# Kernel tuning notes

Hardware: AMD Instinct MI355X
Metric: run time of the kernel (lower is better)

The kernel has to match this reference:

```python
import jax, jax.numpy as jnp
import numpy as np

N, E, DN, DE, H = 50000, 800000, 64, 64, 128


def setup_inputs() -> dict:
    key = jax.random.key(0)
    ks = jax.random.split(key, 12)
    s = 0.05
    return {
        "h": jax.random.normal(ks[0], (N, DN), jnp.float32),
        "eh": jax.random.normal(ks[1], (E, DE), jnp.float32),
        "W_node1": jax.random.normal(ks[2], (DN, H), jnp.float32) * s,
        "b_node1": jax.random.normal(ks[3], (H,), jnp.float32) * s,
        "W_node2": jax.random.normal(ks[4], (H, H), jnp.float32) * s,
        "W_edge1": jax.random.normal(ks[5], (DE, H), jnp.float32) * s,
        "b_edge1": jax.random.normal(ks[6], (H,), jnp.float32) * s,
        "W_edge2": jax.random.normal(ks[7], (H, H), jnp.float32) * s,
        "W_comb": jax.random.normal(ks[8], (H, DN), jnp.float32) * s,
        "W_ue": jax.random.normal(ks[9], (DN, DE), jnp.float32) * s,
        "src": jax.random.randint(ks[10], (E,), 0, N, jnp.int32),
        "dst": jax.random.randint(ks[11], (E,), 0, N, jnp.int32),
    }


def reference(h, eh, W_node1, b_node1, W_node2, W_edge1, b_edge1, W_edge2, W_comb, W_ue, src, dst):
    # gather per-edge endpoint node features: [E, DN]
    hs = h[src]
    hd = h[dst]
    # edge update: h_e = 0.8*h_e + 0.2 * fc_update_edge(h_src * h_dst)
    eh_new = 0.8 * eh + 0.2 * ((hs * hd) @ W_ue)
    # message: two small MLPs then tanh-combine, all per edge
    m1 = jax.nn.relu(hs @ W_node1 + b_node1) @ W_node2       # [E, H]
    m2 = jax.nn.relu(eh_new @ W_edge1 + b_edge1) @ W_edge2   # [E, H]
    m = jnp.tanh((m1 * m2) @ W_comb)                          # [E, DN]
    # reduce: scatter-sum messages to destination nodes + residual
    agg = jax.ops.segment_sum(m, dst, num_segments=h.shape[0])
    return agg + h
```

## Files before the change

### kernel.cpp

```cpp
#include <hip/hip_runtime.h>
#include <hip/hip_bf16.h>

#define NN 50000
#define NE 800000
#define DNODE 64
#define HD 128

typedef __attribute__((ext_vector_type(8)))  short bf16x8;
typedef __attribute__((ext_vector_type(16))) float f32x16;
typedef __attribute__((ext_vector_type(4)))  float f32x4;

__device__ __forceinline__ short f2bf(float f) {
    __hip_bfloat16 b = __float2bfloat16(f);
    unsigned short u;
    __builtin_memcpy(&u, &b, 2);
    return (short)u;
}
__device__ __forceinline__ float bf2f(short s) {
    return __uint_as_float(((unsigned)(unsigned short)s) << 16);
}
__device__ __forceinline__ f32x16 zero16() {
    f32x16 z;
#pragma unroll
    for (int i = 0; i < 16; ++i) z[i] = 0.f;
    return z;
}

__device__ __forceinline__ void build_frags(const float* __restrict__ W, int ncols,
                                            int nks, int nct, bf16x8* dst,
                                            int tid, int nthr) {
    int total = nct * nks * 64;
    for (int p = tid; p < total; p += nthr) {
        int fi = p >> 6, l = p & 63;
        int ct = fi / nks, ks = fi - ct * nks;
        int col = 32 * ct + (l & 31);
        int kb  = 16 * ks + 8 * (l >> 5);
        bf16x8 v;
#pragma unroll
        for (int j = 0; j < 8; ++j) v[j] = f2bf(W[(size_t)(kb + j) * ncols + col]);
        dst[p] = v;
    }
}

__global__ __launch_bounds__(512, 2) void node_kernel(
        const float* __restrict__ h, const float* __restrict__ Wn1,
        const float* __restrict__ bn1, const float* __restrict__ Wn2,
        unsigned short* __restrict__ M1, float* __restrict__ out, int ntiles) {
    __shared__ bf16x8 fWn1[16 * 64];
    __shared__ bf16x8 fWn2[32 * 64];
    __shared__ float  bias[HD];
    __shared__ __align__(16) char stg[8][8192];

    int tid = threadIdx.x;
    build_frags(Wn1, HD, 4, 4, fWn1, tid, 512);
    build_frags(Wn2, HD, 8, 4, fWn2, tid, 512);
    if (tid < HD) bias[tid] = bn1[tid];
    __syncthreads();

    int wv = tid >> 6, lane = tid & 63;
    int la = lane & 31, hh = lane >> 5;
    char* stage = stg[wv];

    float bv[4];
#pragma unroll
    for (int ct = 0; ct < 4; ++ct) bv[ct] = bias[32 * ct + la];

    int tile = blockIdx.x * 8 + wv;
    if (tile >= ntiles) return;
    int n0 = tile * 32;
    int nd = n0 + la;
    int ndc = nd < NN ? nd : NN - 1;

    f32x16 accT[4] = {zero16(), zero16(), zero16(), zero16()};
#pragma unroll
    for (int ks = 0; ks < 4; ++ks) {
        int cb = 16 * ks + 8 * hh;
        f32x4 h0 = *(const f32x4*)&h[(size_t)ndc * DNODE + cb];
        f32x4 h1 = *(const f32x4*)&h[(size_t)ndc * DNODE + cb + 4];
        if (nd < NN) {
            *(f32x4*)&out[(size_t)nd * DNODE + cb]     = h0;
            *(f32x4*)&out[(size_t)nd * DNODE + cb + 4] = h1;
        }
        bf16x8 a;
#pragma unroll
        for (int j = 0; j < 4; ++j) { a[j] = f2bf(h0[j]); a[4 + j] = f2bf(h1[j]); }
#pragma unroll
        for (int ct = 0; ct < 4; ++ct)
            accT[ct] = __builtin_amdgcn_mfma_f32_32x32x16_bf16(a, fWn1[(ct * 4 + ks) * 64 + lane], accT[ct], 0, 0, 0);
    }
#pragma unroll
    for (int ct = 0; ct < 4; ++ct)
#pragma unroll
        for (int r = 0; r < 16; ++r) {
            int row = (r & 3) + 8 * (r >> 2) + 4 * hh;
            float v = fmaxf(accT[ct][r] + bv[ct], 0.f);
            int col = 32 * ct + la;
            *(short*)&stage[row * 256 + ((2 * col) ^ ((row & 7) << 4))] = f2bf(v);
        }
    f32x16 accM[4] = {zero16(), zero16(), zero16(), zero16()};
#pragma unroll
    for (int ks = 0; ks < 8; ++ks) {
        int k0 = 16 * ks + 8 * hh;
        bf16x8 a = *(const bf16x8*)&stage[la * 256 + ((2 * k0) ^ ((la & 7) << 4))];
#pragma unroll
        for (int ct = 0; ct < 4; ++ct)
            accM[ct] = __builtin_amdgcn_mfma_f32_32x32x16_bf16(a, fWn2[(ct * 8 + ks) * 64 + lane], accM[ct], 0, 0, 0);
    }
#pragma unroll
    for (int ct = 0; ct < 4; ++ct)
#pragma unroll
        for (int r = 0; r < 16; ++r) {
            int row = (r & 3) + 8 * (r >> 2) + 4 * hh;
            int node = n0 + row;
            if (node < NN)
                M1[(size_t)node * HD + 32 * ct + la] = (unsigned short)f2bf(accM[ct][r]);
        }
}

__global__ __launch_bounds__(512, 2) void edge_kernel(
        const float* __restrict__ h, const float* __restrict__ eh,
        const float* __restrict__ Wue, const float* __restrict__ We1,
        const float* __restrict__ be1, const float* __restrict__ We2,
        const float* __restrict__ Wcb, const int* __restrict__ src,
        const int* __restrict__ dst, const unsigned short* __restrict__ M1,
        float* __restrict__ out) {
    __shared__ bf16x8 fUe[8 * 64];
    __shared__ bf16x8 fE1[16 * 64];
    __shared__ bf16x8 fE2[32 * 64];
    __shared__ bf16x8 fCb[16 * 64];
    __shared__ float  bias[HD];
    __shared__ __align__(16) char stg[8][8192];
    __shared__ int    sdd[8][32];

    int tid = threadIdx.x;
    build_frags(Wue, 64, 4, 2, fUe, tid, 512);
    build_frags(We1, HD, 4, 4, fE1, tid, 512);
    build_frags(We2, HD, 8, 4, fE2, tid, 512);
    build_frags(Wcb, 64, 8, 2, fCb, tid, 512);
    if (tid < HD) bias[tid] = be1[tid];
    __syncthreads();

    int wv = tid >> 6, lane = tid & 63;
    int la = lane & 31, hh = lane >> 5;
    char* stage = stg[wv];

    float bv[4];
#pragma unroll
    for (int ct = 0; ct < 4; ++ct) bv[ct] = bias[32 * ct + la];

    const int NT = NE / 32;
    int gw = blockIdx.x * 8 + wv;
    int t0 = (int)(((long long)gw * NT) >> 11);
    int t1 = (int)(((long long)(gw + 1) * NT) >> 11);

    for (int t = t0; t < t1; ++t) {
        int e0 = t * 32;
        if (lane < 32) sdd[wv][lane] = dst[e0 + lane];
        int srcA = src[e0 + la];
        int dstA = dst[e0 + la];

        int dstD[16];
#pragma unroll
        for (int r = 0; r < 16; ++r)
            dstD[r] = sdd[wv][(r & 3) + 8 * (r >> 2) + 4 * hh];

        float ehv[2][16];
#pragma unroll
        for (int ct = 0; ct < 2; ++ct)
#pragma unroll
            for (int r = 0; r < 16; ++r) {
                int row = (r & 3) + 8 * (r >> 2) + 4 * hh;
                ehv[ct][r] = eh[(size_t)(e0 + row) * 64 + 32 * ct + la];
            }

        bf16x8 mv[8];
#pragma unroll
        for (int ks = 0; ks < 8; ++ks)
            mv[ks] = *(const bf16x8*)((const char*)M1 + (size_t)srcA * 256 + 32 * ks + 16 * hh);

        f32x16 accU[2] = {zero16(), zero16()};
#pragma unroll
        for (int ks = 0; ks < 4; ++ks) {
            int cb = 16 * ks + 8 * hh;
            f32x4 s0 = *(const f32x4*)&h[(size_t)srcA * 64 + cb];
            f32x4 s1 = *(const f32x4*)&h[(size_t)srcA * 64 + cb + 4];
            f32x4 d0 = *(const f32x4*)&h[(size_t)dstA * 64 + cb];
            f32x4 d1 = *(const f32x4*)&h[(size_t)dstA * 64 + cb + 4];
            bf16x8 a;
#pragma unroll
            for (int j = 0; j < 4; ++j) {
                a[j]     = f2bf(s0[j] * d0[j]);
                a[4 + j] = f2bf(s1[j] * d1[j]);
            }
#pragma unroll
            for (int ct = 0; ct < 2; ++ct)
                accU[ct] = __builtin_amdgcn_mfma_f32_32x32x16_bf16(a, fUe[(ct * 4 + ks) * 64 + lane], accU[ct], 0, 0, 0);
        }
#pragma unroll
        for (int ct = 0; ct < 2; ++ct)
#pragma unroll
            for (int r = 0; r < 16; ++r) {
                int row = (r & 3) + 8 * (r >> 2) + 4 * hh;
                float v = 0.8f * ehv[ct][r] + 0.2f * accU[ct][r];
                int col = 32 * ct + la;
                *(short*)&stage[row * 128 + ((2 * col) ^ ((row & 7) << 4))] = f2bf(v);
            }
        f32x16 accT[4] = {zero16(), zero16(), zero16(), zero16()};
#pragma unroll
        for (int ks = 0; ks < 4; ++ks) {
            int k0 = 16 * ks + 8 * hh;
            bf16x8 a = *(const bf16x8*)&stage[la * 128 + ((2 * k0) ^ ((la & 7) << 4))];
#pragma unroll
            for (int ct = 0; ct < 4; ++ct)
                accT[ct] = __builtin_amdgcn_mfma_f32_32x32x16_bf16(a, fE1[(ct * 4 + ks) * 64 + lane], accT[ct], 0, 0, 0);
        }
#pragma unroll
        for (int ct = 0; ct < 4; ++ct)
#pragma unroll
            for (int r = 0; r < 16; ++r) {
                int row = (r & 3) + 8 * (r >> 2) + 4 * hh;
                float v = fmaxf(accT[ct][r] + bv[ct], 0.f);
                int col = 32 * ct + la;
                *(short*)&stage[row * 256 + ((2 * col) ^ ((row & 7) << 4))] = f2bf(v);
            }
        f32x16 accM[4] = {zero16(), zero16(), zero16(), zero16()};
#pragma unroll
        for (int ks = 0; ks < 8; ++ks) {
            int k0 = 16 * ks + 8 * hh;
            bf16x8 a = *(const bf16x8*)&stage[la * 256 + ((2 * k0) ^ ((la & 7) << 4))];
#pragma unroll
            for (int ct = 0; ct < 4; ++ct)
                accM[ct] = __builtin_amdgcn_mfma_f32_32x32x16_bf16(a, fE2[(ct * 8 + ks) * 64 + lane], accM[ct], 0, 0, 0);
        }
#pragma unroll
        for (int ct = 0; ct < 4; ++ct)
#pragma unroll
            for (int r = 0; r < 16; ++r) {
                int row = (r & 3) + 8 * (r >> 2) + 4 * hh;
                int col = 32 * ct + la;
                *(short*)&stage[row * 256 + ((2 * col) ^ ((row & 7) << 4))] = f2bf(accM[ct][r]);
            }
        f32x16 accF[2] = {zero16(), zero16()};
#pragma unroll
        for (int ks = 0; ks < 8; ++ks) {
            int k0 = 16 * ks + 8 * hh;
            bf16x8 m2 = *(const bf16x8*)&stage[la * 256 + ((2 * k0) ^ ((la & 7) << 4))];
            bf16x8 ap;
#pragma unroll
            for (int i = 0; i < 8; ++i)
                ap[i] = f2bf(bf2f(m2[i]) * bf2f(mv[ks][i]));
#pragma unroll
            for (int ct = 0; ct < 2; ++ct)
                accF[ct] = __builtin_amdgcn_mfma_f32_32x32x16_bf16(ap, fCb[(ct * 8 + ks) * 64 + lane], accF[ct], 0, 0, 0);
        }
#pragma unroll
        for (int ct = 0; ct < 2; ++ct)
#pragma unroll
            for (int r = 0; r < 16; ++r) {
                float x = accF[ct][r];
                x = fminf(fmaxf(x, -10.f), 10.f);
                float ex = __expf(2.f * x);
                float m = (ex - 1.f) * __builtin_amdgcn_rcpf(ex + 1.f);
                unsafeAtomicAdd(&out[(size_t)dstD[r] * 64 + 32 * ct + la], m);
            }
    }
}

extern "C" void kernel_launch(void* const* d_in, const int* in_sizes, int n_in,
                              void* d_out, int out_size, void* d_ws, size_t ws_size,
                              hipStream_t stream) {
    const float* h   = (const float*)d_in[0];
    const float* eh  = (const float*)d_in[1];
    const float* Wn1 = (const float*)d_in[2];
    const float* bn1 = (const float*)d_in[3];
    const float* Wn2 = (const float*)d_in[4];
    const float* We1 = (const float*)d_in[5];
    const float* be1 = (const float*)d_in[6];
    const float* We2 = (const float*)d_in[7];
    const float* Wcb = (const float*)d_in[8];
    const float* Wue = (const float*)d_in[9];
    const int*   src = (const int*)d_in[10];
    const int*   dst = (const int*)d_in[11];
    float* out = (float*)d_out;
    unsigned short* M1 = (unsigned short*)d_ws;

    int ntiles = (NN + 31) / 32;
    node_kernel<<<(ntiles + 7) / 8, 512, 0, stream>>>(h, Wn1, bn1, Wn2, M1, out, ntiles);
    edge_kernel<<<256, 512, 0, stream>>>(h, eh, Wue, We1, be1, We2, Wcb, src, dst, M1, out);
}
```

Baseline: 523.5 us.

## Chain MFMA stages through registers with transposed products and permlane swaps

Drops the per-wave LDS staging buffers between MLP layers. Each layer now computes a transposed product (weights as the A operand), and the accumulator is converted straight into the next layer's B fragment using packed bf16 conversion plus v_permlane32_swap. Freeing the LDS raises the occupancy target to 4 blocks per CU, and the edge grid doubles to 512 blocks. eh and M1 are loaded in the transposed layout, and destination indices come from shuffles instead of shared memory. The risk is higher register pressure under the tighter launch bound, which could cause spills.

```diff
diff --git a/kernel.cpp b/kernel.cpp
--- a/kernel.cpp
+++ b/kernel.cpp
@@ -9,6 +9,7 @@
 typedef __attribute__((ext_vector_type(8)))  short bf16x8;
 typedef __attribute__((ext_vector_type(16))) float f32x16;
 typedef __attribute__((ext_vector_type(4)))  float f32x4;
+typedef __attribute__((ext_vector_type(4)))  unsigned short u16x4;
 
 __device__ __forceinline__ short f2bf(float f) {
     __hip_bfloat16 b = __float2bfloat16(f);
@@ -16,14 +17,32 @@
     __builtin_memcpy(&u, &b, 2);
     return (short)u;
 }
-__device__ __forceinline__ float bf2f(short s) {
-    return __uint_as_float(((unsigned)(unsigned short)s) << 16);
+__device__ __forceinline__ float bf2f(unsigned short s) {
+    return __uint_as_float(((unsigned)s) << 16);
 }
 __device__ __forceinline__ f32x16 zero16() {
     f32x16 z;
 #pragma unroll
     for (int i = 0; i < 16; ++i) z[i] = 0.f;
     return z;
+}
+
+__device__ __forceinline__ unsigned cvt_pk(float lo, float hi) {
+    unsigned r;
+    asm("v_cvt_pk_bf16_f32 %0, %1, %2" : "=v"(r) : "v"(lo), "v"(hi));
+    return r;
+}
+
+__device__ __forceinline__ bf16x8 pack_swap(const float* v) {
+    unsigned w0 = cvt_pk(v[0], v[1]);
+    unsigned w1 = cvt_pk(v[2], v[3]);
+    unsigned w2 = cvt_pk(v[4], v[5]);
+    unsigned w3 = cvt_pk(v[6], v[7]);
+    asm("v_permlane32_swap_b32 %0, %1" : "+v"(w0), "+v"(w2));
+    asm("v_permlane32_swap_b32 %0, %1" : "+v"(w1), "+v"(w3));
+    union { unsigned u[4]; bf16x8 f; } o;
+    o.u[0] = w0; o.u[1] = w1; o.u[2] = w2; o.u[3] = w3;
+    return o.f;
 }
 
 __device__ __forceinline__ void build_frags(const float* __restrict__ W, int ncols,
@@ -42,14 +61,13 @@
     }
 }
 
-__global__ __launch_bounds__(512, 2) void node_kernel(
+__global__ __launch_bounds__(512, 4) void node_kernel(
         const float* __restrict__ h, const float* __restrict__ Wn1,
         const float* __restrict__ bn1, const float* __restrict__ Wn2,
         unsigned short* __restrict__ M1, float* __restrict__ out, int ntiles) {
     __shared__ bf16x8 fWn1[16 * 64];
     __shared__ bf16x8 fWn2[32 * 64];
     __shared__ float  bias[HD];
-    __shared__ __align__(16) char stg[8][8192];
 
     int tid = threadIdx.x;
     build_frags(Wn1, HD, 4, 4, fWn1, tid, 512);
@@ -59,65 +77,67 @@
 
     int wv = tid >> 6, lane = tid & 63;
     int la = lane & 31, hh = lane >> 5;
-    char* stage = stg[wv];
-
-    float bv[4];
-#pragma unroll
-    for (int ct = 0; ct < 4; ++ct) bv[ct] = bias[32 * ct + la];
 
     int tile = blockIdx.x * 8 + wv;
     if (tile >= ntiles) return;
     int n0 = tile * 32;
-    int nd = n0 + la;
-    int ndc = nd < NN ? nd : NN - 1;
-
-    f32x16 accT[4] = {zero16(), zero16(), zero16(), zero16()};
+    int n_la = n0 + la;
+    int nc = n_la < NN ? n_la : NN - 1;
+
+    bf16x8 hfrag[4];
 #pragma unroll
     for (int ks = 0; ks < 4; ++ks) {
         int cb = 16 * ks + 8 * hh;
-        f32x4 h0 = *(const f32x4*)&h[(size_t)ndc * DNODE + cb];
-        f32x4 h1 = *(const f32x4*)&h[(size_t)ndc * DNODE + cb + 4];
-        if (nd < NN) {
-            *(f32x4*)&out[(size_t)nd * DNODE + cb]     = h0;
-            *(f32x4*)&out[(size_t)nd * DNODE + cb + 4] = h1;
-        }
-        bf16x8 a;
-#pragma unroll
-        for (int j = 0; j < 4; ++j) { a[j] = f2bf(h0[j]); a[4 + j] = f2bf(h1[j]); }
-#pragma unroll
-        for (int ct = 0; ct < 4; ++ct)
-            accT[ct] = __builtin_amdgcn_mfma_f32_32x32x16_bf16(a, fWn1[(ct * 4 + ks) * 64 + lane], accT[ct], 0, 0, 0);
-    }
-#pragma unroll
-    for (int ct = 0; ct < 4; ++ct)
-#pragma unroll
-        for (int r = 0; r < 16; ++r) {
-            int row = (r & 3) + 8 * (r >> 2) + 4 * hh;
-            float v = fmaxf(accT[ct][r] + bv[ct], 0.f);
-            int col = 32 * ct + la;
-            *(short*)&stage[row * 256 + ((2 * col) ^ ((row & 7) << 4))] = f2bf(v);
-        }
-    f32x16 accM[4] = {zero16(), zero16(), zero16(), zero16()};
-#pragma unroll
-    for (int ks = 0; ks < 8; ++ks) {
-        int k0 = 16 * ks + 8 * hh;
-        bf16x8 a = *(const bf16x8*)&stage[la * 256 + ((2 * k0) ^ ((la & 7) << 4))];
-#pragma unroll
-        for (int ct = 0; ct < 4; ++ct)
-            accM[ct] = __builtin_amdgcn_mfma_f32_32x32x16_bf16(a, fWn2[(ct * 8 + ks) * 64 + lane], accM[ct], 0, 0, 0);
-    }
-#pragma unroll
-    for (int ct = 0; ct < 4; ++ct)
+        f32x4 h0 = *(const f32x4*)&h[(size_t)nc * DNODE + cb];
+        f32x4 h1 = *(const f32x4*)&h[(size_t)nc * DNODE + cb + 4];
+        if (n_la < NN) {
+            *(f32x4*)&out[(size_t)n_la * DNODE + cb]     = h0;
+            *(f32x4*)&out[(size_t)n_la * DNODE + cb + 4] = h1;
+        }
+        union { unsigned u[4]; bf16x8 f; } xf;
+        xf.u[0] = cvt_pk(h0[0], h0[1]);
+        xf.u[1] = cvt_pk(h0[2], h0[3]);
+        xf.u[2] = cvt_pk(h1[0], h1[1]);
+        xf.u[3] = cvt_pk(h1[2], h1[3]);
+        hfrag[ks] = xf.f;
+    }
+
+    bf16x8 tfrag[8];
+#pragma unroll
+    for (int ct = 0; ct < 4; ++ct) {
+        f32x16 acc = zero16();
+#pragma unroll
+        for (int ks = 0; ks < 4; ++ks)
+            acc = __builtin_amdgcn_mfma_f32_32x32x16_bf16(fWn1[(ct * 4 + ks) * 64 + lane], hfrag[ks], acc, 0, 0, 0);
+        float vals[16];
+#pragma unroll
+        for (int m = 0; m < 4; ++m) {
+            f32x4 bv = *(const f32x4*)&bias[32 * ct + 8 * m + 4 * hh];
+#pragma unroll
+            for (int j = 0; j < 4; ++j)
+                vals[4 * m + j] = fmaxf(acc[4 * m + j] + bv[j], 0.f);
+        }
+        tfrag[2 * ct]     = pack_swap(&vals[0]);
+        tfrag[2 * ct + 1] = pack_swap(&vals[8]);
+    }
+
+#pragma unroll
+    for (int ct = 0; ct < 4; ++ct) {
+        f32x16 acc = zero16();
+#pragma unroll
+        for (int ks = 0; ks < 8; ++ks)
+            acc = __builtin_amdgcn_mfma_f32_32x32x16_bf16(tfrag[ks], fWn2[(ct * 8 + ks) * 64 + lane], acc, 0, 0, 0);
 #pragma unroll
         for (int r = 0; r < 16; ++r) {
             int row = (r & 3) + 8 * (r >> 2) + 4 * hh;
             int node = n0 + row;
             if (node < NN)
-                M1[(size_t)node * HD + 32 * ct + la] = (unsigned short)f2bf(accM[ct][r]);
-        }
-}
-
-__global__ __launch_bounds__(512, 2) void edge_kernel(
+                M1[(size_t)node * HD + 32 * ct + la] = (unsigned short)f2bf(acc[r]);
+        }
+    }
+}
+
+__global__ __launch_bounds__(512, 4) void edge_kernel(
         const float* __restrict__ h, const float* __restrict__ eh,
         const float* __restrict__ Wue, const float* __restrict__ We1,
         const float* __restrict__ be1, const float* __restrict__ We2,
@@ -129,8 +149,6 @@
     __shared__ bf16x8 fE2[32 * 64];
     __shared__ bf16x8 fCb[16 * 64];
     __shared__ float  bias[HD];
-    __shared__ __align__(16) char stg[8][8192];
-    __shared__ int    sdd[8][32];
 
     int tid = threadIdx.x;
     build_frags(Wue, 64, 4, 2, fUe, tid, 512);
@@ -142,127 +160,111 @@
 
     int wv = tid >> 6, lane = tid & 63;
     int la = lane & 31, hh = lane >> 5;
-    char* stage = stg[wv];
-
-    float bv[4];
-#pragma unroll
-    for (int ct = 0; ct < 4; ++ct) bv[ct] = bias[32 * ct + la];
 
     const int NT = NE / 32;
     int gw = blockIdx.x * 8 + wv;
-    int t0 = (int)(((long long)gw * NT) >> 11);
-    int t1 = (int)(((long long)(gw + 1) * NT) >> 11);
+    int t0 = (int)(((long long)gw * NT) >> 12);
+    int t1 = (int)(((long long)(gw + 1) * NT) >> 12);
 
     for (int t = t0; t < t1; ++t) {
         int e0 = t * 32;
-        if (lane < 32) sdd[wv][lane] = dst[e0 + lane];
-        int srcA = src[e0 + la];
-        int dstA = dst[e0 + la];
-
-        int dstD[16];
-#pragma unroll
-        for (int r = 0; r < 16; ++r)
-            dstD[r] = sdd[wv][(r & 3) + 8 * (r >> 2) + 4 * hh];
-
-        float ehv[2][16];
-#pragma unroll
-        for (int ct = 0; ct < 2; ++ct)
-#pragma unroll
-            for (int r = 0; r < 16; ++r) {
-                int row = (r & 3) + 8 * (r >> 2) + 4 * hh;
-                ehv[ct][r] = eh[(size_t)(e0 + row) * 64 + 32 * ct + la];
-            }
-
-        bf16x8 mv[8];
-#pragma unroll
-        for (int ks = 0; ks < 8; ++ks)
-            mv[ks] = *(const bf16x8*)((const char*)M1 + (size_t)srcA * 256 + 32 * ks + 16 * hh);
-
-        f32x16 accU[2] = {zero16(), zero16()};
+        int e_la = e0 + la;
+        int srcA = src[e_la];
+        int dstA = dst[e_la];
+
+        f32x16 accU0 = zero16(), accU1 = zero16();
 #pragma unroll
         for (int ks = 0; ks < 4; ++ks) {
             int cb = 16 * ks + 8 * hh;
-            f32x4 s0 = *(const f32x4*)&h[(size_t)srcA * 64 + cb];
-            f32x4 s1 = *(const f32x4*)&h[(size_t)srcA * 64 + cb + 4];
-            f32x4 d0 = *(const f32x4*)&h[(size_t)dstA * 64 + cb];
-            f32x4 d1 = *(const f32x4*)&h[(size_t)dstA * 64 + cb + 4];
-            bf16x8 a;
-#pragma unroll
-            for (int j = 0; j < 4; ++j) {
-                a[j]     = f2bf(s0[j] * d0[j]);
-                a[4 + j] = f2bf(s1[j] * d1[j]);
+            f32x4 s0 = *(const f32x4*)&h[(size_t)srcA * DNODE + cb];
+            f32x4 s1 = *(const f32x4*)&h[(size_t)srcA * DNODE + cb + 4];
+            f32x4 d0 = *(const f32x4*)&h[(size_t)dstA * DNODE + cb];
+            f32x4 d1 = *(const f32x4*)&h[(size_t)dstA * DNODE + cb + 4];
+            union { unsigned u[4]; bf16x8 f; } xf;
+            xf.u[0] = cvt_pk(s0[0] * d0[0], s0[1] * d0[1]);
+            xf.u[1] = cvt_pk(s0[2] * d0[2], s0[3] * d0[3]);
+            xf.u[2] = cvt_pk(s1[0] * d1[0], s1[1] * d1[1]);
+            xf.u[3] = cvt_pk(s1[2] * d1[2], s1[3] * d1[3]);
+            accU0 = __builtin_amdgcn_mfma_f32_32x32x16_bf16(fUe[(0 * 4 + ks) * 64 + lane], xf.f, accU0, 0, 0, 0);
+            accU1 = __builtin_amdgcn_mfma_f32_32x32x16_bf16(fUe[(1 * 4 + ks) * 64 + lane], xf.f, accU1, 0, 0, 0);
+        }
+
+        bf16x8 efrag[4];
+#pragma unroll
+        for (int ct = 0; ct < 2; ++ct) {
+            const f32x16& aU = ct ? accU1 : accU0;
+            float vals[16];
+#pragma unroll
+            for (int m = 0; m < 4; ++m) {
+                f32x4 ev = *(const f32x4*)&eh[(size_t)e_la * 64 + 32 * ct + 8 * m + 4 * hh];
+#pragma unroll
+                for (int j = 0; j < 4; ++j)
+                    vals[4 * m + j] = 0.8f * ev[j] + 0.2f * aU[4 * m + j];
             }
-#pragma unroll
-            for (int ct = 0; ct < 2; ++ct)
-                accU[ct] = __builtin_amdgcn_mfma_f32_32x32x16_bf16(a, fUe[(ct * 4 + ks) * 64 + lane], accU[ct], 0, 0, 0);
-        }
-#pragma unroll
-        for (int ct = 0; ct < 2; ++ct)
+            efrag[2 * ct]     = pack_swap(&vals[0]);
+            efrag[2 * ct + 1] = pack_swap(&vals[8]);
+        }
+
+        bf16x8 tfrag[8];
+#pragma unroll
+        for (int ct = 0; ct < 4; ++ct) {
+            f32x16 acc = zero16();
+#pragma unroll
+            for (int ks = 0; ks < 4; ++ks)
+                acc = __builtin_amdgcn_mfma_f32_32x32x16_bf16(fE1[(ct * 4 + ks) * 64 + lane], efrag[ks], acc, 0, 0, 0);
+            float vals[16];
+#pragma unroll
+            for (int m = 0; m < 4; ++m) {
+                f32x4 bv = *(const f32x4*)&bias[32 * ct + 8 * m + 4 * hh];
+#pragma unroll
+                for (int j = 0; j < 4; ++j)
+                    vals[4 * m + j] = fmaxf(acc[4 * m + j] + bv[j], 0.f);
+            }
+            tfrag[2 * ct]     = pack_swap(&vals[0]);
+            tfrag[2 * ct + 1] = pack_swap(&vals[8]);
+        }
+
+        bf16x8 pfrag[8];
+#pragma unroll
+        for (int ct = 0; ct < 4; ++ct) {
+            u16x4 mq[4];
+#pragma unroll
+            for (int m = 0; m < 4; ++m)
+                mq[m] = *(const u16x4*)&M1[(size_t)srcA * HD + 32 * ct + 8 * m + 4 * hh];
+            f32x16 acc = zero16();
+#pragma unroll
+            for (int ks = 0; ks < 8; ++ks)
+                acc = __builtin_amdgcn_mfma_f32_32x32x16_bf16(fE2[(ct * 8 + ks) * 64 + lane], tfrag[ks], acc, 0, 0, 0);
+            float vals[16];
+#pragma unroll
+            for (int m = 0; m < 4; ++m)
+#pragma unroll
+                for (int j = 0; j < 4; ++j)
+                    vals[4 * m + j] = acc[4 * m + j] * bf2f(mq[m][j]);
+            pfrag[2 * ct]     = pack_swap(&vals[0]);
+            pfrag[2 * ct + 1] = pack_swap(&vals[8]);
+        }
+
+        int dstR[16];
+#pragma unroll
+        for (int r = 0; r < 16; ++r)
+            dstR[r] = __shfl(dstA, (r & 3) + 8 * (r >> 2) + 4 * hh);
+
+#pragma unroll
+        for (int ct = 0; ct < 2; ++ct) {
+            f32x16 acc = zero16();
+#pragma unroll
+            for (int ks = 0; ks < 8; ++ks)
+                acc = __builtin_amdgcn_mfma_f32_32x32x16_bf16(pfrag[ks], fCb[(ct * 8 + ks) * 64 + lane], acc, 0, 0, 0);
 #pragma unroll
             for (int r = 0; r < 16; ++r) {
-                int row = (r & 3) + 8 * (r >> 2) + 4 * hh;
-                float v = 0.8f * ehv[ct][r] + 0.2f * accU[ct][r];
-                int col = 32 * ct + la;
-                *(short*)&stage[row * 128 + ((2 * col) ^ ((row & 7) << 4))] = f2bf(v);
-            }
-        f32x16 accT[4] = {zero16(), zero16(), zero16(), zero16()};
-#pragma unroll
-        for (int ks = 0; ks < 4; ++ks) {
-            int k0 = 16 * ks + 8 * hh;
-            bf16x8 a = *(const bf16x8*)&stage[la * 128 + ((2 * k0) ^ ((la & 7) << 4))];
-#pragma unroll
-            for (int ct = 0; ct < 4; ++ct)
-                accT[ct] = __builtin_amdgcn_mfma_f32_32x32x16_bf16(a, fE1[(ct * 4 + ks) * 64 + lane], accT[ct], 0, 0, 0);
-        }
-#pragma unroll
-        for (int ct = 0; ct < 4; ++ct)
-#pragma unroll
-            for (int r = 0; r < 16; ++r) {
-                int row = (r & 3) + 8 * (r >> 2) + 4 * hh;
-                float v = fmaxf(accT[ct][r] + bv[ct], 0.f);
-                int col = 32 * ct + la;
-                *(short*)&stage[row * 256 + ((2 * col) ^ ((row & 7) << 4))] = f2bf(v);
-            }
-        f32x16 accM[4] = {zero16(), zero16(), zero16(), zero16()};
-#pragma unroll
-        for (int ks = 0; ks < 8; ++ks) {
-            int k0 = 16 * ks + 8 * hh;
-            bf16x8 a = *(const bf16x8*)&stage[la * 256 + ((2 * k0) ^ ((la & 7) << 4))];
-#pragma unroll
-            for (int ct = 0; ct < 4; ++ct)
-                accM[ct] = __builtin_amdgcn_mfma_f32_32x32x16_bf16(a, fE2[(ct * 8 + ks) * 64 + lane], accM[ct], 0, 0, 0);
-        }
-#pragma unroll
-        for (int ct = 0; ct < 4; ++ct)
-#pragma unroll
-            for (int r = 0; r < 16; ++r) {
-                int row = (r & 3) + 8 * (r >> 2) + 4 * hh;
-                int col = 32 * ct + la;
-                *(short*)&stage[row * 256 + ((2 * col) ^ ((row & 7) << 4))] = f2bf(accM[ct][r]);
-            }
-        f32x16 accF[2] = {zero16(), zero16()};
-#pragma unroll
-        for (int ks = 0; ks < 8; ++ks) {
-            int k0 = 16 * ks + 8 * hh;
-            bf16x8 m2 = *(const bf16x8*)&stage[la * 256 + ((2 * k0) ^ ((la & 7) << 4))];
-            bf16x8 ap;
-#pragma unroll
-            for (int i = 0; i < 8; ++i)
-                ap[i] = f2bf(bf2f(m2[i]) * bf2f(mv[ks][i]));
-#pragma unroll
-            for (int ct = 0; ct < 2; ++ct)
-                accF[ct] = __builtin_amdgcn_mfma_f32_32x32x16_bf16(ap, fCb[(ct * 8 + ks) * 64 + lane], accF[ct], 0, 0, 0);
-        }
-#pragma unroll
-        for (int ct = 0; ct < 2; ++ct)
-#pragma unroll
-            for (int r = 0; r < 16; ++r) {
-                float x = accF[ct][r];
+                float x = acc[r];
                 x = fminf(fmaxf(x, -10.f), 10.f);
                 float ex = __expf(2.f * x);
                 float m = (ex - 1.f) * __builtin_amdgcn_rcpf(ex + 1.f);
-                unsafeAtomicAdd(&out[(size_t)dstD[r] * 64 + 32 * ct + la], m);
+                unsafeAtomicAdd(&out[(size_t)dstR[r] * DNODE + 32 * ct + la], m);
             }
+        }
     }
 }
 
@@ -286,5 +288,5 @@
 
     int ntiles = (NN + 31) / 32;
     node_kernel<<<(ntiles + 7) / 8, 512, 0, stream>>>(h, Wn1, bn1, Wn2, M1, out, ntiles);
-    edge_kernel<<<256, 512, 0, stream>>>(h, eh, Wue, We1, be1, We2, Wcb, src, dst, M1, out);
-}
+    edge_kernel<<<512, 512, 0, stream>>>(h, eh, Wue, We1, be1, We2, Wcb, src, dst, M1, out);
+}
```

After: 519.1 us. Within noise of the previous version (-0.8%).
